# Performance work log

Hardware: AMD Instinct MI355X
Metric: run time of the kernel (lower is better)

Reference implementation:

```python
import jax, jax.numpy as jnp
import numpy as np


def setup_inputs() -> dict:
    key = jax.random.key(0)
    ks = jax.random.split(key, 14)
    B, S, C, R = 4, 2048, 1024, 4
    s = 0.02
    inp = {
        "hidden_states": jax.random.normal(ks[0], (B, S, C), jnp.float32),
        "Wq": jax.random.normal(ks[1], (C, C), jnp.float32) * s,
        "Wk": jax.random.normal(ks[2], (C, C), jnp.float32) * s,
        "Wv": jax.random.normal(ks[3], (C, C), jnp.float32) * s,
        "Wo": jax.random.normal(ks[4], (C, C), jnp.float32) * s,
        "bo": jnp.zeros((C,), jnp.float32),
        "q_down": jax.random.normal(ks[5], (R, C), jnp.float32) * (1.0 / R),
        "q_up": jnp.zeros((C, R), jnp.float32) + jax.random.normal(ks[6], (C, R), jnp.float32) * s,
        "k_down": jax.random.normal(ks[7], (R, C), jnp.float32) * (1.0 / R),
        "k_up": jax.random.normal(ks[8], (C, R), jnp.float32) * s,
        "v_down": jax.random.normal(ks[9], (R, C), jnp.float32) * (1.0 / R),
        "v_up": jax.random.normal(ks[10], (C, R), jnp.float32) * s,
        "o_down": jax.random.normal(ks[11], (R, C), jnp.float32) * (1.0 / R),
        "o_up": jax.random.normal(ks[12], (C, R), jnp.float32) * s,
        "num_heads": 16,
    }
    return inp


def _lora_linear(x, W, down, up, scale):
    # base Linear (no bias) + lora_scale * up(down(x))
    base = jnp.einsum("bsc,oc->bso", x, W)
    low = jnp.einsum("bsc,rc->bsr", x, down)
    return base + scale * jnp.einsum("bsr,or->bso", low, up)


def reference(hidden_states, Wq, Wk, Wv, Wo, bo,
              q_down, q_up, k_down, k_up, v_down, v_up, o_down, o_up,
              num_heads):
    B, S, C = hidden_states.shape
    H = num_heads
    D = C // H
    lora_scale = 1.0

    q = _lora_linear(hidden_states, Wq, q_down, q_up, lora_scale)
    k = _lora_linear(hidden_states, Wk, k_down, k_up, lora_scale)
    v = _lora_linear(hidden_states, Wv, v_down, v_up, lora_scale)

    # head_to_batch_dim: [B,S,C] -> [B,H,S,D]
    q = q.reshape(B, S, H, D).transpose(0, 2, 1, 3)
    k = k.reshape(B, S, H, D).transpose(0, 2, 1, 3)
    v = v.reshape(B, S, H, D).transpose(0, 2, 1, 3)

    scale = 1.0 / jnp.sqrt(jnp.asarray(D, hidden_states.dtype))
    scores = jnp.einsum("bhsd,bhtd->bhst", q, k) * scale  # [B,H,S,S]
    probs = jax.nn.softmax(scores, axis=-1)
    out = jnp.einsum("bhst,bhtd->bhsd", probs, v)

    # batch_to_head_dim: [B,H,S,D] -> [B,S,C]
    out = out.transpose(0, 2, 1, 3).reshape(B, S, C)

    out = _lora_linear(out, Wo, o_down, o_up, lora_scale) + bo
    return out
```

## Files before the change

### kernel.cpp

```cpp
#include <hip/hip_runtime.h>
#include <stdint.h>

typedef __attribute__((ext_vector_type(8))) short short8;
typedef __attribute__((ext_vector_type(4))) float f32x4;

typedef const unsigned int __attribute__((address_space(1))) gu32;
typedef unsigned int __attribute__((address_space(3))) lu32;

__device__ __forceinline__ float bf2f(unsigned short u) {
  union { unsigned int i; float f; } v; v.i = ((unsigned int)u) << 16; return v.f;
}
__device__ __forceinline__ unsigned short f2bf(float f) {
  union { float f; unsigned int i; } v; v.f = f;
  unsigned int r = v.i + 0x7FFFu + ((v.i >> 16) & 1u);
  return (unsigned short)(r >> 16);
}
__device__ __forceinline__ float fexp2(float x) {
  float r; asm("v_exp_f32 %0, %1" : "=v"(r) : "v"(x)); return r;
}
__device__ __forceinline__ unsigned int cvtpk(float lo, float hi) {
  unsigned int r;
  asm("v_cvt_pk_bf16_f32 %0, %1, %2" : "=v"(r) : "v"(lo), "v"(hi));
  return r;
}

__global__ __launch_bounds__(256) void prep_in(
    const float* __restrict__ X, unsigned short* __restrict__ Xb,
    const float* __restrict__ Wq, const float* __restrict__ Wk,
    const float* __restrict__ Wv, const float* __restrict__ Wo,
    const float* __restrict__ qd, const float* __restrict__ qu,
    const float* __restrict__ kd, const float* __restrict__ ku,
    const float* __restrict__ vd, const float* __restrict__ vu,
    const float* __restrict__ od, const float* __restrict__ ou,
    unsigned short* __restrict__ Wqkv, unsigned short* __restrict__ Wob)
{
  if (blockIdx.x < 8192) {
    int i = (blockIdx.x * 256 + threadIdx.x) * 4;
    float4 v = *(const float4*)&X[i];
    unsigned long long pk = (unsigned long long)f2bf(v.x) |
                            ((unsigned long long)f2bf(v.y) << 16) |
                            ((unsigned long long)f2bf(v.z) << 32) |
                            ((unsigned long long)f2bf(v.w) << 48);
    *(unsigned long long*)&Xb[i] = pk;
    return;
  }
  int idx = (blockIdx.x - 8192) * 256 + threadIdx.x;
  int sel = idx >> 18;
  int rem = (idx & 0x3FFFF) * 4;
  int o = rem >> 10, c = rem & 1023;
  const float *W, *up, *dn;
  if (sel == 0)      { W = Wq; up = qu; dn = qd; }
  else if (sel == 1) { W = Wk; up = ku; dn = kd; }
  else if (sel == 2) { W = Wv; up = vu; dn = vd; }
  else               { W = Wo; up = ou; dn = od; }
  float4 wv = *(const float4*)&W[rem];
  float a0 = wv.x, a1 = wv.y, a2 = wv.z, a3 = wv.w;
  #pragma unroll
  for (int r = 0; r < 4; r++) {
    float u = up[o * 4 + r];
    float4 dv = *(const float4*)&dn[r * 1024 + c];
    a0 += u * dv.x; a1 += u * dv.y; a2 += u * dv.z; a3 += u * dv.w;
  }
  unsigned long long pk = (unsigned long long)f2bf(a0) |
                          ((unsigned long long)f2bf(a1) << 16) |
                          ((unsigned long long)f2bf(a2) << 32) |
                          ((unsigned long long)f2bf(a3) << 48);
  if (sel < 3) *(unsigned long long*)&Wqkv[sel * 1048576 + rem] = pk;
  else         *(unsigned long long*)&Wob[rem] = pk;
}

template <int OUTF>
__global__ __launch_bounds__(256) void gemm_bt(
    const unsigned short* __restrict__ A, const unsigned short* __restrict__ B,
    unsigned short* __restrict__ Cb, float* __restrict__ Cf,
    const float* __restrict__ bias, unsigned short* __restrict__ Kswz,
    unsigned short* __restrict__ VTs, int M, int N, int K)
{
  __shared__ unsigned short smA[3][128 * 32];
  __shared__ unsigned short smB[3][128 * 32];
  const int tid = threadIdx.x;
  const int w = tid >> 6, lane = tid & 63;
  const int g = lane >> 4, lr = lane & 15;
  const int m0 = blockIdx.y * 128, n0 = blockIdx.x * 128;
  const int srow = lane >> 2;
  const int scol = (lane & 3) * 8;
  const unsigned short* gA = A + (size_t)(m0 + w * 16 + srow) * K + scol;
  const unsigned short* gB = B + (size_t)(n0 + w * 16 + srow) * K + scol;
  f32x4 acc[4][4] = {};
  const int wr = (w >> 1) * 64, wc = (w & 1) * 64;

  auto stage = [&](int buf, int k0) {
    #pragma unroll
    for (int i = 0; i < 2; i++) {
      __builtin_amdgcn_global_load_lds((gu32*)(gA + (size_t)i * 64 * K + k0),
          (lu32*)&smA[buf][(i * 64 + w * 16) * 32], 16, 0, 0);
      __builtin_amdgcn_global_load_lds((gu32*)(gB + (size_t)i * 64 * K + k0),
          (lu32*)&smB[buf][(i * 64 + w * 16) * 32], 16, 0, 0);
    }
  };
  auto compute = [&](int buf) {
    short8 a[4], b[4];
    #pragma unroll
    for (int mi = 0; mi < 4; mi++) a[mi] = *(const short8*)&smA[buf][(wr + mi * 16 + lr) * 32 + g * 8];
    #pragma unroll
    for (int ni = 0; ni < 4; ni++) b[ni] = *(const short8*)&smB[buf][(wc + ni * 16 + lr) * 32 + g * 8];
    #pragma unroll
    for (int mi = 0; mi < 4; mi++)
      #pragma unroll
      for (int ni = 0; ni < 4; ni++)
        acc[mi][ni] = __builtin_amdgcn_mfma_f32_16x16x32_bf16(a[mi], b[ni], acc[mi][ni], 0, 0, 0);
  };

  const int nt = K / 32;
  stage(0, 0);
  stage(1, 32);
  int cur = 0;
  for (int t = 0; t + 2 < nt; ++t) {
    asm volatile("s_waitcnt vmcnt(4)" ::: "memory");
    __builtin_amdgcn_sched_barrier(0);
    __builtin_amdgcn_s_barrier();
    __builtin_amdgcn_sched_barrier(0);
    int nb = (cur == 0) ? 2 : cur - 1;
    stage(nb, (t + 2) * 32);
    compute(cur);
    asm volatile("s_waitcnt lgkmcnt(0)" ::: "memory");
    __builtin_amdgcn_sched_barrier(0);
    cur = (cur == 2) ? 0 : cur + 1;
  }
  asm volatile("s_waitcnt vmcnt(4)" ::: "memory");
  __builtin_amdgcn_sched_barrier(0);
  __builtin_amdgcn_s_barrier();
  __builtin_amdgcn_sched_barrier(0);
  compute(cur);
  asm volatile("s_waitcnt lgkmcnt(0)" ::: "memory");
  __builtin_amdgcn_sched_barrier(0);
  cur = (cur == 2) ? 0 : cur + 1;
  asm volatile("s_waitcnt vmcnt(0)" ::: "memory");
  __builtin_amdgcn_sched_barrier(0);
  __builtin_amdgcn_s_barrier();
  __builtin_amdgcn_sched_barrier(0);
  compute(cur);

  #pragma unroll
  for (int mi = 0; mi < 4; mi++) {
    #pragma unroll
    for (int ni = 0; ni < 4; ni++) {
      int col = n0 + wc + ni * 16 + lr;
      if (OUTF == 0) {
        int sec = col >> 10;
        #pragma unroll
        for (int j = 0; j < 4; j++) {
          int row = m0 + wr + mi * 16 + g * 4 + j;
          unsigned short ov = f2bf(acc[mi][ni][j]);
          int b_ = row >> 11, s = row & 2047;
          if (sec == 0) {
            Cb[(size_t)row * 3072 + col] = ov;
          } else if (sec == 1) {
            int ck = col - 1024, h = ck >> 6, d = ck & 63;
            Kswz[((size_t)(b_ * 16 + h) * 2048 + s) * 64 + (d ^ ((s & 7) << 3))] = ov;
          } else {
            int ck = col - 2048, h = ck >> 6, d = ck & 63;
            VTs[((size_t)((b_ * 16 + h) * 64 + d)) * 2048 +
                (s & ~63) + ((s & 63) ^ ((d & 7) << 3))] = ov;
          }
        }
      } else {
        #pragma unroll
        for (int j = 0; j < 4; j++) {
          int row = m0 + wr + mi * 16 + g * 4 + j;
          Cf[(size_t)row * N + col] = acc[mi][ni][j] + bias[col];
        }
      }
    }
  }
}

__global__ __launch_bounds__(512, 4) void attn(
    const unsigned short* __restrict__ QKV,
    const unsigned short* __restrict__ Kswz,
    const unsigned short* __restrict__ VTs,
    unsigned short* __restrict__ O)
{
  __shared__ unsigned short smK[3][64 * 64];
  __shared__ unsigned short smV[3][64 * 64];
  __shared__ unsigned short smP[8][32 * 64];
  int bh = blockIdx.x, qb = blockIdx.y;
  int b = bh >> 4, h = bh & 15;
  int tid = threadIdx.x, w = tid >> 6, lane = tid & 63;
  int g = lane >> 4, lr = lane & 15;
  int q0 = qb * 256 + w * 32;
  const size_t kbse = (size_t)bh * 2048 * 64;
  const size_t vbse = (size_t)bh * 64 * 2048;
  const int srow8 = lane >> 3;
  const int sc8 = (lane & 7) * 8;

  auto stage = [&](int buf, int n0) {
    const unsigned short* gk = &Kswz[kbse + (size_t)(n0 + w * 8 + srow8) * 64 + sc8];
    __builtin_amdgcn_global_load_lds((gu32*)gk, (lu32*)&smK[buf][(w * 8) * 64], 16, 0, 0);
    const unsigned short* gv = &VTs[vbse + (size_t)(w * 8 + srow8) * 2048 + n0 + sc8];
    __builtin_amdgcn_global_load_lds((gu32*)gv, (lu32*)&smV[buf][(w * 8) * 64], 16, 0, 0);
  };

  const float SC = 0.125f * 1.44269504f;
  short8 bq[2][2];
  #pragma unroll
  for (int qf = 0; qf < 2; qf++)
    #pragma unroll
    for (int ks = 0; ks < 2; ks++) {
      short8 v = *(const short8*)&QKV[(size_t)(b * 2048 + q0 + qf * 16 + lr) * 3072 +
                                      h * 64 + ks * 32 + g * 8];
      #pragma unroll
      for (int j = 0; j < 4; j++) {
        float f0 = bf2f((unsigned short)v[2 * j]) * SC;
        float f1 = bf2f((unsigned short)v[2 * j + 1]) * SC;
        ((unsigned int*)&v)[j] = cvtpk(f0, f1);
      }
      bq[qf][ks] = v;
    }

  short8 vones;
  #pragma unroll
  for (int j = 0; j < 8; j++) vones[j] = (short)0x3F80;

  f32x4 acc_o[2][4] = {};
  f32x4 acc_l[2] = {};

  asm volatile("s_waitcnt vmcnt(0)" ::: "memory");
  __builtin_amdgcn_sched_barrier(0);
  stage(0, 0);
  stage(1, 64);

  auto compute = [&](int buf) {
    const unsigned short* K_ = smK[buf];
    const unsigned short* V_ = smV[buf];
    f32x4 s[4][2] = {};
    __builtin_amdgcn_s_setprio(1);
    #pragma unroll
    for (int nf = 0; nf < 4; nf++) {
      int row = nf * 16 + lr;
      #pragma unroll
      for (int ks = 0; ks < 2; ks++) {
        int eo = (ks * 64 + g * 16) ^ ((row & 7) << 4);
        short8 ak = *(const short8*)&K_[row * 64 + (eo >> 1)];
        #pragma unroll
        for (int qf = 0; qf < 2; qf++)
          s[nf][qf] = __builtin_amdgcn_mfma_f32_16x16x32_bf16(ak, bq[qf][ks], s[nf][qf], 0, 0, 0);
      }
    }
    __builtin_amdgcn_s_setprio(0);

    #pragma unroll
    for (int qf = 0; qf < 2; qf++) {
      int q = qf * 16 + lr;
      #pragma unroll
      for (int nf = 0; nf < 4; nf++) {
        float p0 = fexp2(s[nf][qf][0]);
        float p1 = fexp2(s[nf][qf][1]);
        float p2 = fexp2(s[nf][qf][2]);
        float p3 = fexp2(s[nf][qf][3]);
        uint2 pw;
        pw.x = cvtpk(p0, p1);
        pw.y = cvtpk(p2, p3);
        int eo = ((nf * 16 + g * 4) * 2) ^ ((q & 7) << 4);
        *(uint2*)&smP[w][q * 64 + (eo >> 1)] = pw;
      }
    }

    __builtin_amdgcn_s_setprio(1);
    #pragma unroll
    for (int ks = 0; ks < 2; ks++) {
      short8 ap[2];
      #pragma unroll
      for (int mq = 0; mq < 2; mq++) {
        int q = mq * 16 + lr;
        int eo = (ks * 64 + g * 16) ^ ((q & 7) << 4);
        ap[mq] = *(const short8*)&smP[w][q * 64 + (eo >> 1)];
        acc_l[mq] = __builtin_amdgcn_mfma_f32_16x16x32_bf16(ap[mq], vones, acc_l[mq], 0, 0, 0);
      }
      #pragma unroll
      for (int df = 0; df < 4; df++) {
        int d = df * 16 + lr;
        int eo = (ks * 64 + g * 16) ^ ((d & 7) << 4);
        short8 bv = *(const short8*)&V_[d * 64 + (eo >> 1)];
        #pragma unroll
        for (int mq = 0; mq < 2; mq++)
          acc_o[mq][df] = __builtin_amdgcn_mfma_f32_16x16x32_bf16(ap[mq], bv, acc_o[mq][df], 0, 0, 0);
      }
    }
    __builtin_amdgcn_s_setprio(0);
  };

  int cur = 0;
  for (int t = 0; t + 2 < 32; ++t) {
    asm volatile("s_waitcnt vmcnt(2)" ::: "memory");
    __builtin_amdgcn_sched_barrier(0);
    __builtin_amdgcn_s_barrier();
    __builtin_amdgcn_sched_barrier(0);
    int nb = (cur == 0) ? 2 : cur - 1;
    stage(nb, (t + 2) * 64);
    compute(cur);
    asm volatile("s_waitcnt lgkmcnt(0)" ::: "memory");
    __builtin_amdgcn_sched_barrier(0);
    cur = (cur == 2) ? 0 : cur + 1;
  }
  asm volatile("s_waitcnt vmcnt(2)" ::: "memory");
  __builtin_amdgcn_sched_barrier(0);
  __builtin_amdgcn_s_barrier();
  __builtin_amdgcn_sched_barrier(0);
  compute(cur);
  asm volatile("s_waitcnt lgkmcnt(0)" ::: "memory");
  __builtin_amdgcn_sched_barrier(0);
  cur = (cur == 2) ? 0 : cur + 1;
  asm volatile("s_waitcnt vmcnt(0)" ::: "memory");
  __builtin_amdgcn_sched_barrier(0);
  __builtin_amdgcn_s_barrier();
  __builtin_amdgcn_sched_barrier(0);
  compute(cur);

  #pragma unroll
  for (int mq = 0; mq < 2; mq++)
    #pragma unroll
    for (int j = 0; j < 4; j++) {
      float inv = 1.0f / acc_l[mq][j];
      #pragma unroll
      for (int df = 0; df < 4; df++) {
        int row = b * 2048 + q0 + mq * 16 + g * 4 + j;
        int col = h * 64 + df * 16 + lr;
        O[(size_t)row * 1024 + col] = f2bf(acc_o[mq][df][j] * inv);
      }
    }
}

extern "C" void kernel_launch(void* const* d_in, const int* in_sizes, int n_in,
                              void* d_out, int out_size, void* d_ws, size_t ws_size,
                              hipStream_t stream) {
  const float* X  = (const float*)d_in[0];
  const float* Wq = (const float*)d_in[1];
  const float* Wk = (const float*)d_in[2];
  const float* Wv = (const float*)d_in[3];
  const float* Wo = (const float*)d_in[4];
  const float* bo = (const float*)d_in[5];
  const float* qd = (const float*)d_in[6];
  const float* qu = (const float*)d_in[7];
  const float* kd = (const float*)d_in[8];
  const float* ku = (const float*)d_in[9];
  const float* vd = (const float*)d_in[10];
  const float* vu = (const float*)d_in[11];
  const float* od = (const float*)d_in[12];
  const float* ou = (const float*)d_in[13];

  char* ws = (char*)d_ws;
  unsigned short* Wqkv = (unsigned short*)(ws);
  unsigned short* Wob  = (unsigned short*)(ws + 6291456);
  unsigned short* Xb   = (unsigned short*)(ws + 8388608);
  unsigned short* QKV  = (unsigned short*)(ws + 25165824);
  unsigned short* Kswz = (unsigned short*)(ws + 75497472);
  unsigned short* VTs  = (unsigned short*)(ws + 92274688);

  prep_in<<<12288, 256, 0, stream>>>(X, Xb, Wq, Wk, Wv, Wo, qd, qu, kd, ku,
                                     vd, vu, od, ou, Wqkv, Wob);
  gemm_bt<0><<<dim3(24, 64), 256, 0, stream>>>(Xb, Wqkv, QKV, nullptr, nullptr,
                                               Kswz, VTs, 8192, 3072, 1024);
  attn<<<dim3(64, 8), 512, 0, stream>>>(QKV, Kswz, VTs, Xb);
  gemm_bt<1><<<dim3(8, 64), 256, 0, stream>>>(Xb, Wob, nullptr, (float*)d_out, bo,
                                              nullptr, nullptr, 8192, 1024, 1024);
}
```

Measured before the change: 193.8 us.

## Add 256x256-tile 8-wave QKV GEMM with phased LDS pipeline and swizzle

Replaces the templated 128x128 QKV projection GEMM with a dedicated 512-thread kernel that computes 256x256 output tiles using K-steps of 64. Loads are issued in quarters into a double-buffered, XOR-swizzled LDS layout and interleaved with MFMA phases separated by barriers, with setprio raised around the matrix ops. The goal is more operand reuse per byte loaded and better overlap of global-to-LDS traffic with compute. In exchange it uses more registers and LDS per block, launches fewer blocks (384), and relies on hand-tuned waitcnt ordering. The output projection moves into a non-templated copy of the old kernel.

Result: slower. 197.7 us (+2.0%).

```diff
diff --git a/kernel.cpp b/kernel.cpp
--- a/kernel.cpp
+++ b/kernel.cpp
@@ -69,12 +69,145 @@
   else         *(unsigned long long*)&Wob[rem] = pk;
 }
 
-template <int OUTF>
-__global__ __launch_bounds__(256) void gemm_bt(
+__global__ __launch_bounds__(512, 2) void gemm_qkv8(
     const unsigned short* __restrict__ A, const unsigned short* __restrict__ B,
-    unsigned short* __restrict__ Cb, float* __restrict__ Cf,
-    const float* __restrict__ bias, unsigned short* __restrict__ Kswz,
-    unsigned short* __restrict__ VTs, int M, int N, int K)
+    unsigned short* __restrict__ Cb, unsigned short* __restrict__ Kswz,
+    unsigned short* __restrict__ VTs)
+{
+  const int K = 1024;
+  __shared__ unsigned short smA[2][2][128 * 64];
+  __shared__ unsigned short smB[2][2][128 * 64];
+  const int tid = threadIdx.x;
+  const int w = tid >> 6, lane = tid & 63;
+  const int g = lane >> 4, lr = lane & 15;
+  const int wm = w >> 2, wn = w & 3;
+  const int m0 = blockIdx.y * 256, n0 = blockIdx.x * 256;
+  const int l8 = lane >> 3;
+  const int c8 = (lane & 7) ^ l8;
+  const unsigned short* gA = A + (size_t)(m0 + w * 16 + l8) * K + c8 * 8;
+  const unsigned short* gB = B + (size_t)(n0 + w * 16 + l8) * K + c8 * 8;
+  const int ldsOff = w * 1024;
+
+  f32x4 acc[8][4] = {};
+  short8 af[4][2], bf0[2][2], bf1[2][2];
+
+  auto STG = [&](int d, int h, int kk) {
+    if (h < 2) {
+      const unsigned short* s = gA + (size_t)h * 128 * K + kk;
+      __builtin_amdgcn_global_load_lds((gu32*)s, (lu32*)&smA[d][h][ldsOff], 16, 0, 0);
+      __builtin_amdgcn_global_load_lds((gu32*)(s + (size_t)8 * K), (lu32*)&smA[d][h][ldsOff + 512], 16, 0, 0);
+    } else {
+      const unsigned short* s = gB + (size_t)(h - 2) * 128 * K + kk;
+      __builtin_amdgcn_global_load_lds((gu32*)s, (lu32*)&smB[d][h - 2][ldsOff], 16, 0, 0);
+      __builtin_amdgcn_global_load_lds((gu32*)(s + (size_t)8 * K), (lu32*)&smB[d][h - 2][ldsOff + 512], 16, 0, 0);
+    }
+  };
+  auto LDA = [&](int d, int h2) {
+    #pragma unroll
+    for (int mi2 = 0; mi2 < 4; mi2++)
+      #pragma unroll
+      for (int ks = 0; ks < 2; ks++) {
+        int row = h2 * 64 + mi2 * 16 + lr;
+        af[mi2][ks] = *(const short8*)&smA[d][wm][row * 64 + (((g + ks * 4) ^ (lr & 7))) * 8];
+      }
+  };
+  auto LDB = [&](int d, int n2, short8 bf[2][2]) {
+    #pragma unroll
+    for (int ni2 = 0; ni2 < 2; ni2++)
+      #pragma unroll
+      for (int ks = 0; ks < 2; ks++) {
+        int row = (wn & 1) * 64 + (n2 * 2 + ni2) * 16 + lr;
+        bf[ni2][ks] = *(const short8*)&smB[d][wn >> 1][row * 64 + (((g + ks * 4) ^ (lr & 7))) * 8];
+      }
+  };
+  auto MM = [&](int h2, int n2, short8 bf[2][2]) {
+    __builtin_amdgcn_s_setprio(1);
+    #pragma unroll
+    for (int mi2 = 0; mi2 < 4; mi2++)
+      #pragma unroll
+      for (int ni2 = 0; ni2 < 2; ni2++)
+        #pragma unroll
+        for (int ks = 0; ks < 2; ks++)
+          acc[h2 * 4 + mi2][n2 * 2 + ni2] =
+              __builtin_amdgcn_mfma_f32_16x16x32_bf16(af[mi2][ks], bf[ni2][ks],
+                                                      acc[h2 * 4 + mi2][n2 * 2 + ni2], 0, 0, 0);
+    __builtin_amdgcn_s_setprio(0);
+  };
+
+#define PH_SYNC() do { \
+    __builtin_amdgcn_sched_barrier(0); \
+    __builtin_amdgcn_s_barrier(); \
+    asm volatile("s_waitcnt lgkmcnt(0)" ::: "memory"); \
+    __builtin_amdgcn_sched_barrier(0); } while (0)
+#define PH_END() do { \
+    __builtin_amdgcn_sched_barrier(0); \
+    __builtin_amdgcn_s_barrier(); } while (0)
+
+  STG(0, 2, 0); STG(0, 3, 0); STG(0, 0, 0); STG(0, 1, 0);
+  STG(1, 2, 64); STG(1, 3, 64);
+  asm volatile("s_waitcnt vmcnt(4)" ::: "memory");
+  __builtin_amdgcn_sched_barrier(0);
+  __builtin_amdgcn_s_barrier();
+  __builtin_amdgcn_sched_barrier(0);
+
+  for (int i = 0; i < 8; ++i) {
+    int kA1 = ((2 * i + 1) & 15) * 64;
+    int k02 = ((2 * i + 2) & 15) * 64;
+    int k13 = ((2 * i + 3) & 15) * 64;
+    LDA(0, 0); LDB(0, 0, bf0); STG(1, 0, kA1);
+    PH_SYNC(); MM(0, 0, bf0); PH_END();
+    LDB(0, 1, bf1); STG(1, 1, kA1);
+    PH_SYNC(); MM(0, 1, bf1); PH_END();
+    LDA(0, 1); STG(0, 2, k02);
+    PH_SYNC(); MM(1, 0, bf0); PH_END();
+    STG(0, 3, k02);
+    asm volatile("s_waitcnt vmcnt(4)" ::: "memory");
+    PH_SYNC(); MM(1, 1, bf1); PH_END();
+    LDA(1, 0); LDB(1, 0, bf0); STG(0, 0, k02);
+    PH_SYNC(); MM(0, 0, bf0); PH_END();
+    LDB(1, 1, bf1); STG(0, 1, k02);
+    PH_SYNC(); MM(0, 1, bf1); PH_END();
+    LDA(1, 1); STG(1, 2, k13);
+    PH_SYNC(); MM(1, 0, bf0); PH_END();
+    STG(1, 3, k13);
+    asm volatile("s_waitcnt vmcnt(4)" ::: "memory");
+    PH_SYNC(); MM(1, 1, bf1); PH_END();
+  }
+  asm volatile("s_waitcnt vmcnt(0)" ::: "memory");
+  __builtin_amdgcn_sched_barrier(0);
+
+#undef PH_SYNC
+#undef PH_END
+
+  const int sec = (n0 >> 10);
+  #pragma unroll
+  for (int mi = 0; mi < 8; mi++) {
+    #pragma unroll
+    for (int ni = 0; ni < 4; ni++) {
+      int col = n0 + wn * 64 + ni * 16 + lr;
+      #pragma unroll
+      for (int j = 0; j < 4; j++) {
+        int row = m0 + wm * 128 + mi * 16 + g * 4 + j;
+        unsigned short ov = f2bf(acc[mi][ni][j]);
+        int b_ = row >> 11, s = row & 2047;
+        if (sec == 0) {
+          Cb[(size_t)row * 3072 + col] = ov;
+        } else if (sec == 1) {
+          int ck = col - 1024, h = ck >> 6, d = ck & 63;
+          Kswz[((size_t)(b_ * 16 + h) * 2048 + s) * 64 + (d ^ ((s & 7) << 3))] = ov;
+        } else {
+          int ck = col - 2048, h = ck >> 6, d = ck & 63;
+          VTs[((size_t)((b_ * 16 + h) * 64 + d)) * 2048 +
+              (s & ~63) + ((s & 63) ^ ((d & 7) << 3))] = ov;
+        }
+      }
+    }
+  }
+}
+
+__global__ __launch_bounds__(256) void gemm_o(
+    const unsigned short* __restrict__ A, const unsigned short* __restrict__ B,
+    float* __restrict__ Cf, const float* __restrict__ bias, int M, int N, int K)
 {
   __shared__ unsigned short smA[3][128 * 32];
   __shared__ unsigned short smB[3][128 * 32];
@@ -146,30 +279,10 @@
     #pragma unroll
     for (int ni = 0; ni < 4; ni++) {
       int col = n0 + wc + ni * 16 + lr;
-      if (OUTF == 0) {
-        int sec = col >> 10;
-        #pragma unroll
-        for (int j = 0; j < 4; j++) {
-          int row = m0 + wr + mi * 16 + g * 4 + j;
-          unsigned short ov = f2bf(acc[mi][ni][j]);
-          int b_ = row >> 11, s = row & 2047;
-          if (sec == 0) {
-            Cb[(size_t)row * 3072 + col] = ov;
-          } else if (sec == 1) {
-            int ck = col - 1024, h = ck >> 6, d = ck & 63;
-            Kswz[((size_t)(b_ * 16 + h) * 2048 + s) * 64 + (d ^ ((s & 7) << 3))] = ov;
-          } else {
-            int ck = col - 2048, h = ck >> 6, d = ck & 63;
-            VTs[((size_t)((b_ * 16 + h) * 64 + d)) * 2048 +
-                (s & ~63) + ((s & 63) ^ ((d & 7) << 3))] = ov;
-          }
-        }
-      } else {
-        #pragma unroll
-        for (int j = 0; j < 4; j++) {
-          int row = m0 + wr + mi * 16 + g * 4 + j;
-          Cf[(size_t)row * N + col] = acc[mi][ni][j] + bias[col];
-        }
+      #pragma unroll
+      for (int j = 0; j < 4; j++) {
+        int row = m0 + wr + mi * 16 + g * 4 + j;
+        Cf[(size_t)row * N + col] = acc[mi][ni][j] + bias[col];
       }
     }
   }
@@ -359,9 +472,8 @@
 
   prep_in<<<12288, 256, 0, stream>>>(X, Xb, Wq, Wk, Wv, Wo, qd, qu, kd, ku,
                                      vd, vu, od, ou, Wqkv, Wob);
-  gemm_bt<0><<<dim3(24, 64), 256, 0, stream>>>(Xb, Wqkv, QKV, nullptr, nullptr,
-                                               Kswz, VTs, 8192, 3072, 1024);
+  gemm_qkv8<<<dim3(12, 32), 512, 0, stream>>>(Xb, Wqkv, QKV, Kswz, VTs);
   attn<<<dim3(64, 8), 512, 0, stream>>>(QKV, Kswz, VTs, Xb);
-  gemm_bt<1><<<dim3(8, 64), 256, 0, stream>>>(Xb, Wob, nullptr, (float*)d_out, bo,
-                                              nullptr, nullptr, 8192, 1024, 1024);
-}
+  gemm_o<<<dim3(8, 64), 256, 0, stream>>>(Xb, Wob, (float*)d_out, bo,
+                                          8192, 1024, 1024);
+}
```

## Stage V-transpose epilogue through LDS and swap GEMM grid axes

Applied to the files above, without the earlier changes.

The QKV GEMM epilogue for the V section now writes the tile to shared memory (padded stride 130), then each thread gathers a transposed swizzled row and emits 16-byte vector stores to VTs. Previously each lane scattered 2-byte stores. The branch is now uniform per block (n0), not per column. The grid is also transposed so blockIdx.x walks M tiles, which changes rasterisation and L2 reuse of weight tiles. The costs are extra LDS traffic, two barriers, and 2-byte LDS reads with a possible bank conflict pattern.

After: 179.2 us. 7.5% less time.

```diff
diff --git a/kernel.cpp b/kernel.cpp
--- a/kernel.cpp
+++ b/kernel.cpp
@@ -76,12 +76,13 @@
     const float* __restrict__ bias, unsigned short* __restrict__ Kswz,
     unsigned short* __restrict__ VTs, int M, int N, int K)
 {
-  __shared__ unsigned short smA[3][128 * 32];
-  __shared__ unsigned short smB[3][128 * 32];
+  __shared__ unsigned short sm[24576];
+  unsigned short* smA = sm;
+  unsigned short* smB = sm + 12288;
   const int tid = threadIdx.x;
   const int w = tid >> 6, lane = tid & 63;
   const int g = lane >> 4, lr = lane & 15;
-  const int m0 = blockIdx.y * 128, n0 = blockIdx.x * 128;
+  const int m0 = blockIdx.x * 128, n0 = blockIdx.y * 128;
   const int srow = lane >> 2;
   const int scol = (lane & 3) * 8;
   const unsigned short* gA = A + (size_t)(m0 + w * 16 + srow) * K + scol;
@@ -93,17 +94,17 @@
     #pragma unroll
     for (int i = 0; i < 2; i++) {
       __builtin_amdgcn_global_load_lds((gu32*)(gA + (size_t)i * 64 * K + k0),
-          (lu32*)&smA[buf][(i * 64 + w * 16) * 32], 16, 0, 0);
+          (lu32*)&smA[buf * 4096 + (i * 64 + w * 16) * 32], 16, 0, 0);
       __builtin_amdgcn_global_load_lds((gu32*)(gB + (size_t)i * 64 * K + k0),
-          (lu32*)&smB[buf][(i * 64 + w * 16) * 32], 16, 0, 0);
+          (lu32*)&smB[buf * 4096 + (i * 64 + w * 16) * 32], 16, 0, 0);
     }
   };
   auto compute = [&](int buf) {
     short8 a[4], b[4];
     #pragma unroll
-    for (int mi = 0; mi < 4; mi++) a[mi] = *(const short8*)&smA[buf][(wr + mi * 16 + lr) * 32 + g * 8];
-    #pragma unroll
-    for (int ni = 0; ni < 4; ni++) b[ni] = *(const short8*)&smB[buf][(wc + ni * 16 + lr) * 32 + g * 8];
+    for (int mi = 0; mi < 4; mi++) a[mi] = *(const short8*)&smA[buf * 4096 + (wr + mi * 16 + lr) * 32 + g * 8];
+    #pragma unroll
+    for (int ni = 0; ni < 4; ni++) b[ni] = *(const short8*)&smB[buf * 4096 + (wc + ni * 16 + lr) * 32 + g * 8];
     #pragma unroll
     for (int mi = 0; mi < 4; mi++)
       #pragma unroll
@@ -141,36 +142,70 @@
   __builtin_amdgcn_sched_barrier(0);
   compute(cur);
 
-  #pragma unroll
-  for (int mi = 0; mi < 4; mi++) {
-    #pragma unroll
-    for (int ni = 0; ni < 4; ni++) {
-      int col = n0 + wc + ni * 16 + lr;
-      if (OUTF == 0) {
-        int sec = col >> 10;
-        #pragma unroll
-        for (int j = 0; j < 4; j++) {
-          int row = m0 + wr + mi * 16 + g * 4 + j;
-          unsigned short ov = f2bf(acc[mi][ni][j]);
-          int b_ = row >> 11, s = row & 2047;
-          if (sec == 0) {
-            Cb[(size_t)row * 3072 + col] = ov;
-          } else if (sec == 1) {
-            int ck = col - 1024, h = ck >> 6, d = ck & 63;
-            Kswz[((size_t)(b_ * 16 + h) * 2048 + s) * 64 + (d ^ ((s & 7) << 3))] = ov;
-          } else {
-            int ck = col - 2048, h = ck >> 6, d = ck & 63;
-            VTs[((size_t)((b_ * 16 + h) * 64 + d)) * 2048 +
-                (s & ~63) + ((s & 63) ^ ((d & 7) << 3))] = ov;
-          }
-        }
-      } else {
+  if (OUTF == 1) {
+    #pragma unroll
+    for (int mi = 0; mi < 4; mi++)
+      #pragma unroll
+      for (int ni = 0; ni < 4; ni++) {
+        int col = n0 + wc + ni * 16 + lr;
         #pragma unroll
         for (int j = 0; j < 4; j++) {
           int row = m0 + wr + mi * 16 + g * 4 + j;
           Cf[(size_t)row * N + col] = acc[mi][ni][j] + bias[col];
         }
       }
+    return;
+  }
+
+  if (n0 < 2048) {
+    #pragma unroll
+    for (int mi = 0; mi < 4; mi++)
+      #pragma unroll
+      for (int ni = 0; ni < 4; ni++) {
+        int col = n0 + wc + ni * 16 + lr;
+        #pragma unroll
+        for (int j = 0; j < 4; j++) {
+          int row = m0 + wr + mi * 16 + g * 4 + j;
+          unsigned short ov = f2bf(acc[mi][ni][j]);
+          if (n0 >= 1024) {
+            int b_ = row >> 11, s = row & 2047;
+            int ck = col - 1024, h = ck >> 6, d = ck & 63;
+            Kswz[((size_t)(b_ * 16 + h) * 2048 + s) * 64 + (d ^ ((s & 7) << 3))] = ov;
+          } else {
+            Cb[(size_t)row * 3072 + col] = ov;
+          }
+        }
+      }
+    return;
+  }
+
+  __syncthreads();
+  unsigned short* vbuf = sm;
+  #pragma unroll
+  for (int mi = 0; mi < 4; mi++)
+    #pragma unroll
+    for (int ni = 0; ni < 4; ni++)
+      #pragma unroll
+      for (int j = 0; j < 4; j++) {
+        int r = wr + mi * 16 + g * 4 + j;
+        int c = wc + ni * 16 + lr;
+        vbuf[r * 130 + c] = f2bf(acc[mi][ni][j]);
+      }
+  __syncthreads();
+  {
+    int b_ = m0 >> 11, s0g = m0 & 2047;
+    int ck0 = n0 - 2048;
+    int dd = tid >> 1, shalf = tid & 1;
+    int d = dd & 63, h = (ck0 >> 6) + (dd >> 6);
+    size_t rowbase = ((size_t)(b_ * 16 + h) * 64 + d) * 2048;
+    #pragma unroll
+    for (int gp = 0; gp < 8; gp++) {
+      int gs = gp ^ (d & 7);
+      short8 o;
+      #pragma unroll
+      for (int j = 0; j < 8; j++)
+        o[j] = (short)vbuf[(shalf * 64 + gs * 8 + j) * 130 + dd];
+      *(short8*)&VTs[rowbase + s0g + shalf * 64 + gp * 8] = o;
     }
   }
 }
@@ -359,9 +394,9 @@
 
   prep_in<<<12288, 256, 0, stream>>>(X, Xb, Wq, Wk, Wv, Wo, qd, qu, kd, ku,
                                      vd, vu, od, ou, Wqkv, Wob);
-  gemm_bt<0><<<dim3(24, 64), 256, 0, stream>>>(Xb, Wqkv, QKV, nullptr, nullptr,
+  gemm_bt<0><<<dim3(64, 24), 256, 0, stream>>>(Xb, Wqkv, QKV, nullptr, nullptr,
                                                Kswz, VTs, 8192, 3072, 1024);
   attn<<<dim3(64, 8), 512, 0, stream>>>(QKV, Kswz, VTs, Xb);
-  gemm_bt<1><<<dim3(8, 64), 256, 0, stream>>>(Xb, Wob, nullptr, (float*)d_out, bo,
+  gemm_bt<1><<<dim3(64, 8), 256, 0, stream>>>(Xb, Wob, nullptr, (float*)d_out, bo,
                                               nullptr, nullptr, 8192, 1024, 1024);
 }
```
